# Performance work log

Hardware: AMD Instinct MI355X
Metric: run time of the kernel (lower is better)

Reference implementation:

```python
import jax, jax.numpy as jnp
import numpy as np

BN_EPS = 1e-5
TAU = 1.0  # gumbel temperature

def setup_inputs() -> dict:
    key = jax.random.key(0)
    ks = jax.random.split(key, 6)
    B, O, F, H, HID = 32, 4096, 256, 8, 128
    x = jax.random.normal(ks[0], (B, O, F), dtype=jnp.float32)
    gumbel_noise = jax.random.gumbel(ks[1], (B, O, H), dtype=jnp.float32)
    W_in = jax.random.normal(ks[2], (F, HID), dtype=jnp.float32) * (1.0 / np.sqrt(F))
    b_in = jnp.zeros((HID,), jnp.float32)
    W_blk = jax.random.normal(ks[3], (HID, HID), dtype=jnp.float32) * (1.0 / np.sqrt(HID))
    b_blk = jnp.zeros((HID,), jnp.float32)
    bn_gamma = jnp.ones((HID,), jnp.float32)
    bn_beta = jnp.zeros((HID,), jnp.float32)
    W_fc = jax.random.normal(ks[4], (HID, H), dtype=jnp.float32) * (1.0 / np.sqrt(HID))
    b_fc = jnp.zeros((H,), jnp.float32)
    return {"x": x, "gumbel_noise": gumbel_noise, "W_in": W_in, "b_in": b_in,
            "W_blk": W_blk, "b_blk": b_blk, "bn_gamma": bn_gamma, "bn_beta": bn_beta,
            "W_fc": W_fc, "b_fc": b_fc}

def reference(x, gumbel_noise, W_in, b_in, W_blk, b_blk, bn_gamma, bn_beta, W_fc, b_fc):
    B, O, F = x.shape
    xf = x.reshape(B * O, F)
    # DynamicNetwork head: input linear + relu, one residual block (Linear+BN+ReLU), fc
    h = jax.nn.relu(xf @ W_in + b_in)  # (B*O, HID)
    z = h @ W_blk + b_blk
    mu = z.mean(axis=0)
    var = z.var(axis=0)  # biased var, matches BatchNorm training normalization
    z = (z - mu) * jax.lax.rsqrt(var + BN_EPS) * bn_gamma + bn_beta
    h = jax.nn.relu(z) + h  # residual
    logits = (h @ W_fc + b_fc).reshape(B, O, -1)  # (B, O, H)
    # mask out zero-norm observations
    mask = (jnp.linalg.norm(x, axis=2) != 0)[..., None].astype(x.dtype)  # (B, O, 1)
    logits = logits * mask
    # gumbel softmax over observation dim (soft)
    w = jax.nn.softmax((logits + gumbel_noise) / TAU, axis=1)  # (B, O, H)
    # weighted sum pooling: algebraically the repeat-multiply-sum in the original
    pooled = jnp.einsum('boh,bof->bhf', w, x)  # (B, H, F)
    return pooled.reshape(B, -1)  # (B, H*F)
```

## Files before the change

kernel.cpp:

```cpp
#include <hip/hip_runtime.h>
#include <math.h>

#define MB_ 131072
#define F_  256
#define HID_ 128
#define H_  8
#define O_  4096
#define B_  32

typedef __attribute__((ext_vector_type(8))) short short8;
typedef __attribute__((ext_vector_type(4))) float f32x4;

static __device__ __forceinline__ unsigned short f2bf(float f) {
    unsigned int u = __float_as_uint(f);
    unsigned int r = (u + 0x7fffu + ((u >> 16) & 1u)) >> 16;
    return (unsigned short)r;
}
static __device__ __forceinline__ float bflo(unsigned int u) {
    return __uint_as_float(u << 16);
}
static __device__ __forceinline__ float bfhi(unsigned int u) {
    return __uint_as_float(u & 0xffff0000u);
}
static __device__ __forceinline__ unsigned int fkey(float f) {
    unsigned int u = __float_as_uint(f);
    return (u & 0x80000000u) ? ~u : (u | 0x80000000u);
}
static __device__ __forceinline__ short8 pack_bf16x8(const float4 a, const float4 b) {
    short8 r;
    r[0] = (short)f2bf(a.x); r[1] = (short)f2bf(a.y);
    r[2] = (short)f2bf(a.z); r[3] = (short)f2bf(a.w);
    r[4] = (short)f2bf(b.x); r[5] = (short)f2bf(b.y);
    r[6] = (short)f2bf(b.z); r[7] = (short)f2bf(b.w);
    return r;
}
static __device__ __forceinline__ void gll16(const float* g, float* l) {
    __builtin_amdgcn_global_load_lds(
        (const __attribute__((address_space(1))) float*)g,
        (__attribute__((address_space(3))) float*)l, 16, 0, 0);
}

__global__ __launch_bounds__(256) void k_prep(
    const float* __restrict__ W_in, const float* __restrict__ W_blk,
    unsigned short* __restrict__ WinT, unsigned short* __restrict__ WblkT,
    unsigned int* __restrict__ Mmax)
{
    const int idx = blockIdx.x * 256 + threadIdx.x;
    if (idx < 256) Mmax[idx] = 0u;
    if (idx < 32768) {
        const int n = idx >> 8, k = idx & 255;
        WinT[idx] = f2bf(W_in[(size_t)k * HID_ + n]);
    } else {
        const int i2 = idx - 32768;
        const int n = i2 >> 7, k = i2 & 127;
        WblkT[i2] = f2bf(W_blk[(size_t)k * HID_ + n]);
    }
}

__global__ __launch_bounds__(512, 4) void k_fused(
    const float* __restrict__ x, const unsigned short* __restrict__ WinT,
    const float* __restrict__ b_in,
    const unsigned short* __restrict__ WblkT, const float* __restrict__ b_blk,
    unsigned short* __restrict__ h_out, unsigned short* __restrict__ z_out,
    float* __restrict__ mask_out,
    float* __restrict__ sumP, float* __restrict__ sumsqP)
{
    __shared__ unsigned short smem[16384];
    float* stgf = (float*)smem;
    unsigned short* h_s = smem;

    const int tid = threadIdx.x;
    const int R0 = blockIdx.x * 128;
    const int wave = tid >> 6;
    const int wrow = wave >> 2;
    const int wcol = wave & 3;
    const int lane = tid & 63;
    const int lm = lane & 15, quad = lane >> 4;

    const int r0s = wave * 16 + (lane >> 3);
    const int r1s = r0s + 8;
    const int cl0 = (lane & 7) ^ (r0s & 7);
    const int cl1 = (lane & 7) ^ (r1s & 7);
    const float* g0 = x + (size_t)(R0 + r0s) * F_ + cl0 * 4;
    const float* g1 = x + (size_t)(R0 + r1s) * F_ + cl1 * 4;
    const int lbase = wave * 512;

    int aoff[4][2];
#pragma unroll
    for (int mi = 0; mi < 4; mi++) {
        const int ar = wrow * 64 + mi * 16 + lm;
        aoff[mi][0] = ar * 32 + (((2 * quad) ^ (ar & 7)) << 2);
        aoff[mi][1] = ar * 32 + (((2 * quad + 1) ^ (ar & 7)) << 2);
    }
    const unsigned short* wr0 = WinT + (size_t)(wcol * 32 + lm) * F_ + quad * 8;
    const unsigned short* wr1 = wr0 + (size_t)16 * F_;

    f32x4 acc[4][2];
#pragma unroll
    for (int i = 0; i < 4; i++)
#pragma unroll
        for (int j = 0; j < 2; j++) acc[i][j] = (f32x4){0.f, 0.f, 0.f, 0.f};
    float msq[4] = {0.f, 0.f, 0.f, 0.f};

    gll16(g0, stgf + lbase);
    gll16(g1, stgf + lbase + 256);
    asm volatile("s_waitcnt vmcnt(0)" ::: "memory");
    __builtin_amdgcn_s_barrier();
    __builtin_amdgcn_sched_barrier(0);

#pragma unroll
    for (int kt = 0; kt < 8; kt++) {
        const int b = kt & 1;
        const short8 bC0 = *(const short8*)(wr0 + kt * 32);
        const short8 bC1 = *(const short8*)(wr1 + kt * 32);
        if (kt < 7) {
            float* d = stgf + (b ^ 1) * 4096 + lbase;
            gll16(g0 + (kt + 1) * 32, d);
            gll16(g1 + (kt + 1) * 32, d + 256);
        }
        short8 af[4];
#pragma unroll
        for (int mi = 0; mi < 4; mi++) {
            const float4 fa = *(const float4*)(stgf + b * 4096 + aoff[mi][0]);
            const float4 fb = *(const float4*)(stgf + b * 4096 + aoff[mi][1]);
            if (wcol == 0)
                msq[mi] += fa.x * fa.x + fa.y * fa.y + fa.z * fa.z + fa.w * fa.w
                         + fb.x * fb.x + fb.y * fb.y + fb.z * fb.z + fb.w * fb.w;
            af[mi] = pack_bf16x8(fa, fb);
        }
#pragma unroll
        for (int mi = 0; mi < 4; mi++) {
            acc[mi][0] = __builtin_amdgcn_mfma_f32_16x16x32_bf16(af[mi], bC0, acc[mi][0], 0, 0, 0);
            acc[mi][1] = __builtin_amdgcn_mfma_f32_16x16x32_bf16(af[mi], bC1, acc[mi][1], 0, 0, 0);
        }
        asm volatile("s_waitcnt vmcnt(0)" ::: "memory");
        __builtin_amdgcn_s_barrier();
        __builtin_amdgcn_sched_barrier(0);
    }

    if (wcol == 0) {
#pragma unroll
        for (int mi = 0; mi < 4; mi++) {
            float m = msq[mi];
            m += __shfl_xor(m, 16, 64);
            m += __shfl_xor(m, 32, 64);
            if (quad == 0)
                mask_out[R0 + wrow * 64 + mi * 16 + lm] = (m != 0.f) ? 1.f : 0.f;
        }
    }
    __syncthreads();

    {
        float bcol[2];
#pragma unroll
        for (int ni = 0; ni < 2; ni++) bcol[ni] = b_in[wcol * 32 + ni * 16 + lm];
#pragma unroll
        for (int mi = 0; mi < 4; mi++)
#pragma unroll
            for (int r = 0; r < 4; r++) {
                const int rl = wrow * 64 + mi * 16 + quad * 4 + r;
#pragma unroll
                for (int ni = 0; ni < 2; ni++) {
                    const int col = wcol * 32 + ni * 16 + lm;
                    const float v = fmaxf(acc[mi][ni][r] + bcol[ni], 0.f);
                    h_s[rl * 128 + ((((col >> 3) ^ (rl & 7)) << 3) | (col & 7))] = f2bf(v);
                }
            }
    }
#pragma unroll
    for (int i = 0; i < 4; i++)
#pragma unroll
        for (int j = 0; j < 2; j++) acc[i][j] = (f32x4){0.f, 0.f, 0.f, 0.f};
    __syncthreads();

    {
        const int crow = tid >> 2, cb = tid & 3;
#pragma unroll
        for (int j = 0; j < 4; j++) {
            const int ch = cb * 4 + j;
            const short8 v = *(const short8*)(h_s + crow * 128 + ((ch ^ (crow & 7)) << 3));
            *(short8*)(h_out + (size_t)(R0 + crow) * HID_ + ch * 8) = v;
        }
    }

    {
        const unsigned short* wb0 = WblkT + (size_t)(wcol * 32 + lm) * HID_ + quad * 8;
        const unsigned short* wb1 = wb0 + (size_t)16 * HID_;
#pragma unroll
        for (int kt2 = 0; kt2 < 4; kt2++) {
            short8 wbf[2];
            wbf[0] = *(const short8*)(wb0 + kt2 * 32);
            wbf[1] = *(const short8*)(wb1 + kt2 * 32);
            short8 haf[4];
#pragma unroll
            for (int mi = 0; mi < 4; mi++) {
                const int hr = wrow * 64 + mi * 16 + lm;
                haf[mi] = *(const short8*)(h_s + hr * 128 + (((kt2 * 4 + quad) ^ (hr & 7)) << 3));
            }
#pragma unroll
            for (int mi = 0; mi < 4; mi++)
#pragma unroll
                for (int ni = 0; ni < 2; ni++)
                    acc[mi][ni] = __builtin_amdgcn_mfma_f32_16x16x32_bf16(haf[mi], wbf[ni], acc[mi][ni], 0, 0, 0);
        }
    }

    __syncthreads();

    {
        float bcol2[2];
#pragma unroll
        for (int ni = 0; ni < 2; ni++) bcol2[ni] = b_blk[wcol * 32 + ni * 16 + lm];
        float s_c[2] = {0.f, 0.f}, ss_c[2] = {0.f, 0.f};
#pragma unroll
        for (int mi = 0; mi < 4; mi++)
#pragma unroll
            for (int r = 0; r < 4; r++) {
                const int rl = wrow * 64 + mi * 16 + quad * 4 + r;
#pragma unroll
                for (int ni = 0; ni < 2; ni++) {
                    const int col = wcol * 32 + ni * 16 + lm;
                    const float zv = acc[mi][ni][r] + bcol2[ni];
                    s_c[ni] += zv;
                    ss_c[ni] += zv * zv;
                    h_s[rl * 128 + ((((col >> 3) ^ (rl & 7)) << 3) | (col & 7))] = f2bf(zv);
                }
            }
#pragma unroll
        for (int ni = 0; ni < 2; ni++) {
            s_c[ni]  += __shfl_xor(s_c[ni], 16, 64);
            s_c[ni]  += __shfl_xor(s_c[ni], 32, 64);
            ss_c[ni] += __shfl_xor(ss_c[ni], 16, 64);
            ss_c[ni] += __shfl_xor(ss_c[ni], 32, 64);
        }
        if (quad == 0) {
#pragma unroll
            for (int ni = 0; ni < 2; ni++) {
                const int col = wcol * 32 + ni * 16 + lm;
                sumP[((size_t)blockIdx.x * 2 + wrow) * 128 + col]   = s_c[ni];
                sumsqP[((size_t)blockIdx.x * 2 + wrow) * 128 + col] = ss_c[ni];
            }
        }
    }
    __syncthreads();

    {
        const int crow = tid >> 2, cb = tid & 3;
#pragma unroll
        for (int j = 0; j < 4; j++) {
            const int ch = cb * 4 + j;
            const short8 v = *(const short8*)(h_s + crow * 128 + ((ch ^ (crow & 7)) << 3));
            *(short8*)(z_out + (size_t)(R0 + crow) * HID_ + ch * 8) = v;
        }
    }
}

__global__ __launch_bounds__(256) void k_bnfin(
    const float* __restrict__ sumP, const float* __restrict__ sumsqP,
    const float* __restrict__ gamma, const float* __restrict__ beta,
    float* __restrict__ scale, float* __restrict__ shift)
{
    const int c = blockIdx.x;
    const int tid = threadIdx.x;
    float s = 0.f, ss = 0.f;
    for (int i = tid; i < 2048; i += 256) {
        s  += sumP[(size_t)i * 128 + c];
        ss += sumsqP[(size_t)i * 128 + c];
    }
#pragma unroll
    for (int off = 32; off; off >>= 1) {
        s  += __shfl_xor(s, off, 64);
        ss += __shfl_xor(ss, off, 64);
    }
    __shared__ float rs[4], rss[4];
    const int wid = tid >> 6, lane = tid & 63;
    if (lane == 0) { rs[wid] = s; rss[wid] = ss; }
    __syncthreads();
    if (tid == 0) {
        const float S  = rs[0] + rs[1] + rs[2] + rs[3];
        const float SS = rss[0] + rss[1] + rss[2] + rss[3];
        const float inv_m = 1.0f / (float)MB_;
        const float mu = S * inv_m;
        const float var = SS * inv_m - mu * mu;
        const float sc = gamma[c] * rsqrtf(var + 1e-5f);
        scale[c] = sc;
        shift[c] = beta[c] - mu * sc;
    }
}

__global__ __launch_bounds__(256) void k_logits(
    const unsigned short* __restrict__ h_in, const unsigned short* __restrict__ z_in,
    const float* __restrict__ scale, const float* __restrict__ shift,
    const float* __restrict__ W_fc, const float* __restrict__ b_fc,
    const float* __restrict__ mask, const float* __restrict__ gumbel,
    float* __restrict__ t_out, unsigned int* __restrict__ Mmax)
{
    __shared__ float wfc_s[1024];
    __shared__ float sc_s[128], sh_s[128];
    const int tid = threadIdx.x;
    for (int i = tid; i < 1024; i += 256) wfc_s[i] = W_fc[i];
    if (tid < 128) { sc_s[tid] = scale[tid]; sh_s[tid] = shift[tid]; }
    __syncthreads();

    const size_t row0 = (size_t)blockIdx.x * 512 + tid;
    const size_t row1 = row0 + 256;
    float a0[8], a1[8];
#pragma unroll
    for (int j = 0; j < 8; j++) { a0[j] = 0.f; a1[j] = 0.f; }

    const uint4* hp0 = (const uint4*)(h_in + row0 * HID_);
    const uint4* zq0 = (const uint4*)(z_in + row0 * HID_);
    const uint4* hp1 = (const uint4*)(h_in + row1 * HID_);
    const uint4* zq1 = (const uint4*)(z_in + row1 * HID_);

#pragma unroll 2
    for (int kc = 0; kc < 16; kc++) {
        const uint4 h0 = hp0[kc], z0 = zq0[kc];
        const uint4 h1 = hp1[kc], z1 = zq1[kc];
        const unsigned int hs0[4] = {h0.x, h0.y, h0.z, h0.w};
        const unsigned int zs0[4] = {z0.x, z0.y, z0.z, z0.w};
        const unsigned int hs1[4] = {h1.x, h1.y, h1.z, h1.w};
        const unsigned int zs1[4] = {z1.x, z1.y, z1.z, z1.w};
#pragma unroll
        for (int p = 0; p < 4; p++) {
            const int k = kc * 8 + p * 2;
            const float sck0 = sc_s[k], shk0 = sh_s[k];
            const float sck1 = sc_s[k + 1], shk1 = sh_s[k + 1];
            const float4 wA = *(const float4*)&wfc_s[k * 8];
            const float4 wB = *(const float4*)&wfc_s[k * 8 + 4];
            const float4 wC = *(const float4*)&wfc_s[k * 8 + 8];
            const float4 wD = *(const float4*)&wfc_s[k * 8 + 12];
            {
                const float hf0 = bflo(hs0[p]), hf1 = bfhi(hs0[p]);
                const float zf0 = bflo(zs0[p]), zf1 = bfhi(zs0[p]);
                const float hb0 = fmaxf(zf0 * sck0 + shk0, 0.f) + hf0;
                const float hb1 = fmaxf(zf1 * sck1 + shk1, 0.f) + hf1;
                a0[0] += hb0 * wA.x + hb1 * wC.x;  a0[1] += hb0 * wA.y + hb1 * wC.y;
                a0[2] += hb0 * wA.z + hb1 * wC.z;  a0[3] += hb0 * wA.w + hb1 * wC.w;
                a0[4] += hb0 * wB.x + hb1 * wD.x;  a0[5] += hb0 * wB.y + hb1 * wD.y;
                a0[6] += hb0 * wB.z + hb1 * wD.z;  a0[7] += hb0 * wB.w + hb1 * wD.w;
            }
            {
                const float hf0 = bflo(hs1[p]), hf1 = bfhi(hs1[p]);
                const float zf0 = bflo(zs1[p]), zf1 = bfhi(zs1[p]);
                const float hb0 = fmaxf(zf0 * sck0 + shk0, 0.f) + hf0;
                const float hb1 = fmaxf(zf1 * sck1 + shk1, 0.f) + hf1;
                a1[0] += hb0 * wA.x + hb1 * wC.x;  a1[1] += hb0 * wA.y + hb1 * wC.y;
                a1[2] += hb0 * wA.z + hb1 * wC.z;  a1[3] += hb0 * wA.w + hb1 * wC.w;
                a1[4] += hb0 * wB.x + hb1 * wD.x;  a1[5] += hb0 * wB.y + hb1 * wD.y;
                a1[6] += hb0 * wB.z + hb1 * wD.z;  a1[7] += hb0 * wB.w + hb1 * wD.w;
            }
        }
    }

    float bf[8];
#pragma unroll
    for (int j = 0; j < 8; j++) bf[j] = b_fc[j];
    const float mk0 = mask[row0], mk1 = mask[row1];
    float g0[8], g1[8];
    *(float4*)&g0[0] = *(const float4*)(gumbel + row0 * 8);
    *(float4*)&g0[4] = *(const float4*)(gumbel + row0 * 8 + 4);
    *(float4*)&g1[0] = *(const float4*)(gumbel + row1 * 8);
    *(float4*)&g1[4] = *(const float4*)(gumbel + row1 * 8 + 4);
    float t0[8], t1[8];
#pragma unroll
    for (int j = 0; j < 8; j++) {
        t0[j] = (a0[j] + bf[j]) * mk0 + g0[j];
        t1[j] = (a1[j] + bf[j]) * mk1 + g1[j];
    }
    *(float4*)(t_out + row0 * 8)     = *(float4*)&t0[0];
    *(float4*)(t_out + row0 * 8 + 4) = *(float4*)&t0[4];
    *(float4*)(t_out + row1 * 8)     = *(float4*)&t1[0];
    *(float4*)(t_out + row1 * 8 + 4) = *(float4*)&t1[4];

    float tm[8];
#pragma unroll
    for (int j = 0; j < 8; j++) tm[j] = fmaxf(t0[j], t1[j]);
#pragma unroll
    for (int off = 32; off; off >>= 1)
#pragma unroll
        for (int j = 0; j < 8; j++) tm[j] = fmaxf(tm[j], __shfl_xor(tm[j], off, 64));
    if ((tid & 63) == 0) {
        const int bb = blockIdx.x >> 3;
#pragma unroll
        for (int j = 0; j < 8; j++) atomicMax(&Mmax[bb * 8 + j], fkey(tm[j]));
    }
}

__global__ __launch_bounds__(256) void k_pool(
    const float* __restrict__ x, const float* __restrict__ t_in,
    const unsigned int* __restrict__ Mmax,
    float* __restrict__ pp, float* __restrict__ zp)
{
    __shared__ float ws_s[8][64];
    __shared__ float M_s[8];
    const int tid = threadIdx.x;
    const int oc = blockIdx.x;
    const int b  = blockIdx.y;
    if (tid < 8) {
        const unsigned int k = Mmax[b * 8 + tid];
        const unsigned int s = (k & 0x80000000u) ? (k & 0x7fffffffu) : ~k;
        M_s[tid] = __uint_as_float(s);
    }
    __syncthreads();
#pragma unroll
    for (int i = tid; i < 512; i += 256) {
        const int ol = i >> 3, hh = i & 7;
        const float tv = t_in[((size_t)b * O_ + oc * 64 + ol) * H_ + hh];
        ws_s[hh][ol] = __expf(tv - M_s[hh]);
    }
    __syncthreads();
    if (tid < 8) {
        float s = 0.f;
        for (int o = 0; o < 64; o++) s += ws_s[tid][o];
        zp[((size_t)oc * 32 + b) * 8 + tid] = s;
    }
    float acc[8];
#pragma unroll
    for (int hh = 0; hh < 8; hh++) acc[hh] = 0.f;
    const float* xp = x + ((size_t)b * O_ + oc * 64) * F_ + tid;
#pragma unroll 4
    for (int o = 0; o < 64; o++) {
        const float xv = xp[(size_t)o * F_];
#pragma unroll
        for (int hh = 0; hh < 8; hh++) acc[hh] += ws_s[hh][o] * xv;
    }
    float* outp = pp + ((size_t)oc * 32 + b) * 2048;
#pragma unroll
    for (int hh = 0; hh < 8; hh++) outp[hh * 256 + tid] = acc[hh];
}

__global__ __launch_bounds__(256) void k_reduce(
    const float* __restrict__ pp, const float* __restrict__ zp,
    float* __restrict__ out)
{
    const int blk = blockIdx.x;
    const int b = blk >> 3, hh = blk & 7;
    const int tid = threadIdx.x;
    __shared__ float invZ_s;
    if (tid < 64) {
        float z = zp[((size_t)tid * 32 + b) * 8 + hh];
#pragma unroll
        for (int off = 32; off; off >>= 1) z += __shfl_xor(z, off, 64);
        if (tid == 0) invZ_s = 1.f / z;
    }
    __syncthreads();
    float s = 0.f;
    const float* p0 = pp + (size_t)b * 2048 + hh * 256 + tid;
#pragma unroll 8
    for (int ocq = 0; ocq < 64; ocq++) s += p0[(size_t)ocq * 65536];
    out[(size_t)b * 2048 + hh * 256 + tid] = s * invZ_s;
}

extern "C" void kernel_launch(void* const* d_in, const int* in_sizes, int n_in,
                              void* d_out, int out_size, void* d_ws, size_t ws_size,
                              hipStream_t stream)
{
    const float* x      = (const float*)d_in[0];
    const float* gumbel = (const float*)d_in[1];
    const float* W_in   = (const float*)d_in[2];
    const float* b_in   = (const float*)d_in[3];
    const float* W_blk  = (const float*)d_in[4];
    const float* b_blk  = (const float*)d_in[5];
    const float* gamma  = (const float*)d_in[6];
    const float* beta   = (const float*)d_in[7];
    const float* W_fc   = (const float*)d_in[8];
    const float* b_fc   = (const float*)d_in[9];
    float* out = (float*)d_out;
    char* ws = (char*)d_ws;

    unsigned short* h_bf  = (unsigned short*)(ws + 0);
    float* pp     = (float*)(ws + 0);
    float* zp     = (float*)(ws + 16777216);
    unsigned short* z_bf  = (unsigned short*)(ws + 33554432);
    float* mask   = (float*)(ws + 67108864);
    float* sumP   = (float*)(ws + 67633152);
    float* sumsqP = (float*)(ws + 68681728);
    float* scale  = (float*)(ws + 69730304);
    float* shift  = (float*)(ws + 69730816);
    float* t_buf  = (float*)(ws + 69731328);
    unsigned int* Mmax = (unsigned int*)(ws + 73925632);
    unsigned short* WinT  = (unsigned short*)(ws + 73926656);
    unsigned short* WblkT = (unsigned short*)(ws + 73992192);

    k_prep<<<192, 256, 0, stream>>>(W_in, W_blk, WinT, WblkT, Mmax);
    k_fused<<<1024, 512, 0, stream>>>(x, WinT, b_in, WblkT, b_blk, h_bf, z_bf, mask, sumP, sumsqP);
    k_bnfin<<<128, 256, 0, stream>>>(sumP, sumsqP, gamma, beta, scale, shift);
    k_logits<<<256, 256, 0, stream>>>(h_bf, z_bf, scale, shift, W_fc, b_fc, mask, gumbel, t_buf, Mmax);
    k_pool<<<dim3(64, 32), 256, 0, stream>>>(x, t_buf, Mmax, pp, zp);
    k_reduce<<<256, 256, 0, stream>>>(pp, zp, out);
}
```

Before: 311.0 us.

## Deepen first GEMM pipeline to a 4-stage LDS ring with preloaded weights

Replaces the double-buffered x staging in the first GEMM with a 4-slot LDS ring that keeps three tiles in flight. Each k-step now waits on a partial vmcnt and a single lgkm-plus-barrier, instead of draining all loads at the end of every step. All eight k-steps of W_in bf16 fragments are loaded into registers up front rather than once per step. The cost is twice the shared memory per block and more registers, so the launch-bounds occupancy hint drops from 4 to 2 blocks per CU. That cuts the latency hiding available from other resident waves.

```diff
diff --git a/kernel.cpp b/kernel.cpp
--- a/kernel.cpp
+++ b/kernel.cpp
@@ -38,6 +38,12 @@
     __builtin_amdgcn_global_load_lds(
         (const __attribute__((address_space(1))) float*)g,
         (__attribute__((address_space(3))) float*)l, 16, 0, 0);
+}
+#define WAITV(N) asm volatile("s_waitcnt vmcnt(" #N ")" ::: "memory")
+static __device__ __forceinline__ void bar_lgkm() {
+    asm volatile("s_waitcnt lgkmcnt(0)" ::: "memory");
+    __builtin_amdgcn_s_barrier();
+    __builtin_amdgcn_sched_barrier(0);
 }
 
 __global__ __launch_bounds__(256) void k_prep(
@@ -57,7 +63,7 @@
     }
 }
 
-__global__ __launch_bounds__(512, 4) void k_fused(
+__global__ __launch_bounds__(512, 2) void k_fused(
     const float* __restrict__ x, const unsigned short* __restrict__ WinT,
     const float* __restrict__ b_in,
     const unsigned short* __restrict__ WblkT, const float* __restrict__ b_blk,
@@ -65,9 +71,8 @@
     float* __restrict__ mask_out,
     float* __restrict__ sumP, float* __restrict__ sumsqP)
 {
-    __shared__ unsigned short smem[16384];
-    float* stgf = (float*)smem;
-    unsigned short* h_s = smem;
+    __shared__ float stgf[16384];
+    unsigned short* h_s = (unsigned short*)stgf;
 
     const int tid = threadIdx.x;
     const int R0 = blockIdx.x * 128;
@@ -92,8 +97,15 @@
         aoff[mi][0] = ar * 32 + (((2 * quad) ^ (ar & 7)) << 2);
         aoff[mi][1] = ar * 32 + (((2 * quad + 1) ^ (ar & 7)) << 2);
     }
+
     const unsigned short* wr0 = WinT + (size_t)(wcol * 32 + lm) * F_ + quad * 8;
     const unsigned short* wr1 = wr0 + (size_t)16 * F_;
+    short8 bC[8][2];
+#pragma unroll
+    for (int kt = 0; kt < 8; kt++) {
+        bC[kt][0] = *(const short8*)(wr0 + kt * 32);
+        bC[kt][1] = *(const short8*)(wr1 + kt * 32);
+    }
 
     f32x4 acc[4][2];
 #pragma unroll
@@ -102,41 +114,49 @@
         for (int j = 0; j < 2; j++) acc[i][j] = (f32x4){0.f, 0.f, 0.f, 0.f};
     float msq[4] = {0.f, 0.f, 0.f, 0.f};
 
-    gll16(g0, stgf + lbase);
-    gll16(g1, stgf + lbase + 256);
-    asm volatile("s_waitcnt vmcnt(0)" ::: "memory");
-    __builtin_amdgcn_s_barrier();
-    __builtin_amdgcn_sched_barrier(0);
-
-#pragma unroll
-    for (int kt = 0; kt < 8; kt++) {
-        const int b = kt & 1;
-        const short8 bC0 = *(const short8*)(wr0 + kt * 32);
-        const short8 bC1 = *(const short8*)(wr1 + kt * 32);
-        if (kt < 7) {
-            float* d = stgf + (b ^ 1) * 4096 + lbase;
-            gll16(g0 + (kt + 1) * 32, d);
-            gll16(g1 + (kt + 1) * 32, d + 256);
-        }
-        short8 af[4];
-#pragma unroll
-        for (int mi = 0; mi < 4; mi++) {
-            const float4 fa = *(const float4*)(stgf + b * 4096 + aoff[mi][0]);
-            const float4 fb = *(const float4*)(stgf + b * 4096 + aoff[mi][1]);
-            if (wcol == 0)
-                msq[mi] += fa.x * fa.x + fa.y * fa.y + fa.z * fa.z + fa.w * fa.w
-                         + fb.x * fb.x + fb.y * fb.y + fb.z * fb.z + fb.w * fb.w;
-            af[mi] = pack_bf16x8(fa, fb);
-        }
-#pragma unroll
-        for (int mi = 0; mi < 4; mi++) {
-            acc[mi][0] = __builtin_amdgcn_mfma_f32_16x16x32_bf16(af[mi], bC0, acc[mi][0], 0, 0, 0);
-            acc[mi][1] = __builtin_amdgcn_mfma_f32_16x16x32_bf16(af[mi], bC1, acc[mi][1], 0, 0, 0);
-        }
-        asm volatile("s_waitcnt vmcnt(0)" ::: "memory");
-        __builtin_amdgcn_s_barrier();
-        __builtin_amdgcn_sched_barrier(0);
-    }
+#pragma unroll
+    for (int t = 0; t < 3; t++) {
+        float* d = stgf + t * 4096 + lbase;
+        gll16(g0 + t * 32, d);
+        gll16(g1 + t * 32, d + 256);
+    }
+
+#define G1STEP(KT, NW)                                                         \
+    {                                                                          \
+        WAITV(NW);               \
+        bar_lgkm();           \
+        if ((KT) < 5) {                 \
+            float* d = stgf + (((KT) + 3) & 3) * 4096 + lbase;                 \
+            gll16(g0 + ((KT) + 3) * 32, d);                                    \
+            gll16(g1 + ((KT) + 3) * 32, d + 256);                              \
+        }                                                                      \
+        const float* sb = stgf + ((KT) & 3) * 4096;                            \
+        short8 af[4];                                                          \
+        _Pragma("unroll")                                                      \
+        for (int mi = 0; mi < 4; mi++) {                                       \
+            const float4 fa = *(const float4*)(sb + aoff[mi][0]);              \
+            const float4 fb = *(const float4*)(sb + aoff[mi][1]);              \
+            if (wcol == 0)                                                     \
+                msq[mi] += fa.x*fa.x + fa.y*fa.y + fa.z*fa.z + fa.w*fa.w       \
+                         + fb.x*fb.x + fb.y*fb.y + fb.z*fb.z + fb.w*fb.w;      \
+            af[mi] = pack_bf16x8(fa, fb);                                      \
+        }                                                                      \
+        _Pragma("unroll")                                                      \
+        for (int mi = 0; mi < 4; mi++) {                                       \
+            acc[mi][0] = __builtin_amdgcn_mfma_f32_16x16x32_bf16(af[mi], bC[KT][0], acc[mi][0], 0, 0, 0); \
+            acc[mi][1] = __builtin_amdgcn_mfma_f32_16x16x32_bf16(af[mi], bC[KT][1], acc[mi][1], 0, 0, 0); \
+        }                                                                      \
+    }
+
+    G1STEP(0, 4)
+    G1STEP(1, 4)
+    G1STEP(2, 4)
+    G1STEP(3, 4)
+    G1STEP(4, 4)
+    G1STEP(5, 4)
+    G1STEP(6, 2)
+    G1STEP(7, 0)
+#undef G1STEP
 
     if (wcol == 0) {
 #pragma unroll
```

Measured after the change: 329.4 us. +5.9%, slower.
